# Kernel tuning notes

Measured on AMD Instinct MI355X. Metric: run time of the kernel, lower is better.

Reference implementation:

```python
import jax, jax.numpy as jnp
import numpy as np

V, L, H, D = 2048, 16, 8, 64   # vocab, max_chars, n_head, word_vec_d
B = 8192                        # number of words in batch (rows of char_code)
NW_TOTAL = 8192                 # len(word_code)
N_NAMES = 2048                  # total names (4 words each)
N_GROUPS = 8                    # groups of names (256 each)
PAD = 0
TEMP = D ** 0.5
LN_EPS = 1e-5


def make_pos():
    freq = D // 2
    inv = 1.0 / np.power(10000.0, np.arange(freq) / freq)
    ph = np.outer(np.arange(L), inv)
    return jnp.asarray(np.hstack([np.cos(ph), np.sin(ph)]).astype(np.float32))


def setup_inputs() -> dict:
    key = jax.random.key(0)
    ks = jax.random.split(key, 8)
    char_emb = jax.random.normal(ks[0], (V, D), jnp.float32) * 0.02
    char_emb = char_emb.at[PAD].set(0.0)  # padding_idx row
    Wc = jax.random.normal(ks[1], (D, 3 * H * D), jnp.float32) * 0.02
    bc = jnp.zeros((3 * H * D,), jnp.float32)
    Wp = jax.random.normal(ks[2], (D, 3 * H * D), jnp.float32) * 0.02
    bp = jnp.zeros((3 * H * D,), jnp.float32)
    gamma = jnp.ones((D,), jnp.float32)
    beta = jnp.zeros((D,), jnp.float32)
    W1 = jax.random.normal(ks[3], (H, 16), jnp.float32) * 0.1
    b1 = jnp.zeros((16,), jnp.float32)
    W2 = jax.random.normal(ks[4], (16, 8), jnp.float32) * 0.1
    b2 = jnp.zeros((8,), jnp.float32)
    char_code = jax.random.randint(ks[5], (B, L), 1, V)
    char_code = char_code.at[::4, -2:].set(PAD)  # some padded tails
    word_code = jax.random.randint(ks[6], (NW_TOTAL,), 0, B)
    n_words = np.full((N_NAMES,), NW_TOTAL // N_NAMES, dtype=np.int64)
    n_names = np.full((N_GROUPS,), N_NAMES // N_GROUPS, dtype=np.int64)
    return {"char_emb": char_emb, "Wc": Wc, "bc": bc, "Wp": Wp, "bp": bp,
            "gamma": gamma, "beta": beta, "W1": W1, "b1": b1, "W2": W2, "b2": b2,
            "char_code": char_code, "word_code": word_code,
            "n_words": n_words, "n_names": n_names}


def reference(char_emb, Wc, bc, Wp, bp, gamma, beta, W1, b1, W2, b2,
              char_code, word_code, n_words, n_names):
    pos = make_pos()
    # ComputeQKV: linear d -> 3*H*d, reshape [N,3,H,D]
    cqkv = (char_emb @ Wc + bc).reshape(V, 3, H, D)
    cq, ck, cv = cqkv[:, 0], cqkv[:, 1], cqkv[:, 2]        # [V,H,D]
    pqkv = (pos @ Wp + bp).reshape(L, 3, H, D)
    pq, pk, pv = pqkv[:, 0], pqkv[:, 1], pqkv[:, 2]        # [L,H,D]
    # precomputed score tables
    char_qk = jnp.einsum('xhd,yhd->hxy', cq, ck).at[:, :, PAD].set(-1e9)  # [H,V,V]
    pos_qk = jnp.einsum('xhd,yhd->hxy', pq, pk)                            # [H,L,L]
    # char_q@pos_k + (pos_q@char_k)^T summed over the first dim of char_pos_qk
    cp = jnp.einsum('vhd,lhd->hvl', cq, pk) + jnp.einsum('lhd,vhd->hvl', pq, ck)  # [H,V,L]
    code = char_code                                        # [B,L]
    # gather-assembled scores, no [H,B*L,V] intermediate
    sim = (char_qk[:, code[:, :, None], code[:, None, :]]   # [H,B,L,L]
           + cp[:, code]
           + pos_qk[:, None]) / TEMP
    attn = jax.nn.softmax(sim, axis=-1)                     # [H,B,L,L] (dropout=0)
    v = jnp.transpose(cv[code], (2, 0, 1, 3)) + pv.transpose(1, 0, 2)[:, None]  # [H,B,L,D]
    out = jnp.einsum('hbij,hbjd->bihd', attn, v)            # [B,L,H,D]
    mu = out.mean(-1, keepdims=True)
    var = out.var(-1, keepdims=True)
    out = (out - mu) / jnp.sqrt(var + LN_EPS) * gamma + beta  # LayerNorm(D)
    char_ft = jnp.transpose(out, (0, 2, 1, 3))              # [B,H,L,D]
    mask = (code != PAD)
    pooled = jnp.einsum('bl,bhld->bhd', mask.astype(out.dtype), char_ft) \
             / mask.sum(-1)[:, None, None]                  # masked mean over chars
    x = jnp.transpose(pooled, (0, 2, 1))                    # [B,D,H]
    x = jax.nn.relu(x @ W1 + b1) @ W2 + b2                  # MLP over head dim -> [B,D,8]
    word_ft = x.reshape(B, -1)[word_code]                   # [NW_TOTAL, D*8]
    nw = np.asarray(n_words)
    seg = jnp.asarray(np.repeat(np.arange(nw.size), nw))
    name_ft = jax.ops.segment_sum(word_ft, seg, num_segments=nw.size) \
              / jnp.asarray(nw, word_ft.dtype)[:, None]     # ragged mean -> [N_NAMES, D*8]
    splits = np.cumsum(np.asarray(n_names))[:-1]
    return tuple(jnp.split(name_ft, splits, axis=0))
```

## Files before the change

kernel.cpp:

```cpp
#include <hip/hip_runtime.h>
#include <hip/hip_bf16.h>
#include <math.h>

typedef __attribute__((ext_vector_type(8))) short bfrag;
typedef __attribute__((ext_vector_type(4))) float ffrag;
typedef __attribute__((ext_vector_type(4))) float f4v;
typedef __attribute__((ext_vector_type(2))) float f2v;

#define C3 1536
#define PS 24
#define VS 136

__device__ __forceinline__ unsigned short f2bf(float f) {
    unsigned u = __float_as_uint(f);
    return (unsigned short)((u + 0x7FFFu + ((u >> 16) & 1u)) >> 16);
}
__device__ __forceinline__ float bf2f(unsigned short u) {
    return __uint_as_float((unsigned)u << 16);
}

__device__ __forceinline__ float row16_sum(float x) {
    int v;
    v = __builtin_amdgcn_update_dpp(0, __float_as_int(x), 0xB1, 0xF, 0xF, true);
    x += __int_as_float(v);
    v = __builtin_amdgcn_update_dpp(0, __float_as_int(x), 0x4E, 0xF, 0xF, true);
    x += __int_as_float(v);
    v = __builtin_amdgcn_update_dpp(0, __float_as_int(x), 0x124, 0xF, 0xF, true);
    x += __int_as_float(v);
    v = __builtin_amdgcn_update_dpp(0, __float_as_int(x), 0x128, 0xF, 0xF, true);
    x += __int_as_float(v);
    return x;
}

__global__ __launch_bounds__(256) void precompute_kernel(
    const float* __restrict__ char_emb, const float* __restrict__ Wc, const float* __restrict__ bc,
    const float* __restrict__ Wp, const float* __restrict__ bp,
    const float* __restrict__ gamma, const float* __restrict__ beta,
    unsigned short* __restrict__ cqkv, unsigned short* __restrict__ pbf,
    unsigned short* __restrict__ pvb, float* __restrict__ gbtab)
{
    const int b = blockIdx.x;
    const int t = threadIdx.x;
    if (b < 1536) {
        const int mt = b / 6;
        const int nt = b - mt * 6;
        const int m0 = mt * 8;
        const int c = nt * 256 + t;
        const float qs = (c < 512) ? 0.125f : 1.f;
        const float bias = bc[c];
        float acc[8];
        #pragma unroll
        for (int r = 0; r < 8; ++r) acc[r] = bias;
        #pragma unroll 16
        for (int dd = 0; dd < 64; ++dd) {
            const float wv = Wc[dd * C3 + c];
            #pragma unroll
            for (int r = 0; r < 8; ++r)
                acc[r] = fmaf(char_emb[(m0 + r) * 64 + dd], wv, acc[r]);
        }
        #pragma unroll
        for (int r = 0; r < 8; ++r)
            cqkv[(size_t)(m0 + r) * C3 + c] = f2bf(acc[r] * qs);
    } else {
        const int e = b - 1536;
        const int l = e / 6;
        const int cc = e - l * 6;
        if (b == 1536 && t < 64) {
            #pragma unroll
            for (int dt = 0; dt < 4; ++dt) {
                gbtab[t * 8 + dt]     = gamma[dt * 16 + t];
                gbtab[t * 8 + 4 + dt] = beta[dt * 16 + t];
            }
        }
        __shared__ float spos[64];
        if (t < 64) {
            const int f = t & 31;
            const float inv = exp2f(-(float)f * 0.41524101186092034f);
            const float ph = (float)l * inv;
            spos[t] = (t < 32) ? cosf(ph) : sinf(ph);
        }
        __syncthreads();
        const int c = t + cc * 256;
        float acc = bp[c];
        #pragma unroll
        for (int dd = 0; dd < 64; ++dd)
            acc = fmaf(spos[dd], Wp[dd * C3 + c], acc);
        if (c < 1024) {
            const float qs = (c < 512) ? 0.125f : 1.f;
            pbf[(c >> 6) * 1024 + l * 64 + (c & 63)] = f2bf(acc * qs);
        } else {
            const int h = (c >> 6) & 7, d = c & 63;
            pvb[((h * 4 + (d >> 4)) * 2 + (l >> 3)) * 128 + (d & 15) * 8 + (l & 7)] = f2bf(acc);
        }
    }
}

__global__ __launch_bounds__(256) void cp_kernel(
    const unsigned short* __restrict__ cqkv, const unsigned short* __restrict__ pbf,
    float* __restrict__ cps, float* __restrict__ pqk)
{
    const int b = blockIdx.x;
    const int t = threadIdx.x;
    if (b < 256) {
        const int lane = t & 63, wid = t >> 6;
        const int quad = lane >> 4, n = lane & 15;
        const int h = b >> 5;
        const int v0 = (b & 31) * 64 + wid * 16;
        const unsigned short* arow = cqkv + (size_t)(v0 + n) * C3 + h * 64;
        const unsigned short* pk = pbf + (8 + h) * 1024 + n * 64;
        const unsigned short* pq = pbf + h * 1024 + n * 64;
        ffrag acc = {0.f, 0.f, 0.f, 0.f};
        #pragma unroll
        for (int s = 0; s < 2; ++s) {
            const bfrag aF = *(const bfrag*)(arow + s * 32 + quad * 8);
            const bfrag bF = *(const bfrag*)(pk + s * 32 + quad * 8);
            acc = __builtin_amdgcn_mfma_f32_16x16x32_bf16(aF, bF, acc, 0, 0, 0);
        }
        #pragma unroll
        for (int s = 0; s < 2; ++s) {
            const bfrag aF = *(const bfrag*)(arow + 512 + s * 32 + quad * 8);
            const bfrag bF = *(const bfrag*)(pq + s * 32 + quad * 8);
            acc = __builtin_amdgcn_mfma_f32_16x16x32_bf16(aF, bF, acc, 0, 0, 0);
        }
        #pragma unroll
        for (int r = 0; r < 4; ++r)
            cps[((size_t)h * 2048 + v0 + quad * 4 + r) * 16 + n] = acc[r];
    } else {
        #pragma unroll
        for (int i = 0; i < 8; ++i) {
            const int e = t * 8 + i;
            const int h = e >> 8, r = (e >> 4) & 15, c = e & 15;
            const unsigned short* pq = pbf + h * 1024 + r * 64;
            const unsigned short* pk = pbf + (8 + h) * 1024 + c * 64;
            float s = 0.f;
            #pragma unroll
            for (int c8 = 0; c8 < 8; ++c8) {
                const bfrag a = *(const bfrag*)(pq + c8 * 8);
                const bfrag bb = *(const bfrag*)(pk + c8 * 8);
                #pragma unroll
                for (int j = 0; j < 8; ++j)
                    s += bf2f((unsigned short)a[j]) * bf2f((unsigned short)bb[j]);
            }
            pqk[e] = s;
        }
    }
}

__global__ __launch_bounds__(256, 7) void attn_kernel(
    const unsigned short* __restrict__ cqkv,
    const unsigned short* __restrict__ pvb, const int* __restrict__ char_code,
    const float* __restrict__ gbtab,
    const float* __restrict__ cps, const float* __restrict__ pqk,
    float* __restrict__ pooled)
{
    __shared__ __attribute__((aligned(16))) unsigned short sVt[4 * 8 * VS];
    __shared__ __attribute__((aligned(16))) unsigned short sP[4 * 16 * PS];

    const int t = threadIdx.x;
    const int lane = t & 63;
    const int wid = t >> 6;
    const int h = blockIdx.x & 7;
    const int w = (blockIdx.x >> 3) * 4 + wid;
    const int quad = lane >> 4;
    const int n = lane & 15;
    const int q2 = quad & 1;

    const int code = char_code[w * 16 + n];
    const bool kvalid = (code != 0);
    const unsigned long long msk = __ballot(kvalid);
    const int nv = __popcll(msk & 0xFFFFull);

    int rc[4];
    #pragma unroll
    for (int rr = 0; rr < 4; ++rr) rc[rr] = __shfl(code, quad * 4 + rr);

    const f4v g4 = *(const f4v*)(gbtab + n * 8);
    const f4v b4 = *(const f4v*)(gbtab + n * 8 + 4);

    unsigned short* vt = sVt + wid * 8 * VS;
    unsigned short* pt = sP + wid * 16 * PS;

    bfrag onesf;
    #pragma unroll
    for (int j = 0; j < 8; ++j) onesf[j] = (short)0x3F80;

    const unsigned short* cvp = cqkv + (size_t)code * C3 + 1024 + h * 64;
    #pragma unroll
    for (int cc = 0; cc < 2; ++cc) {
        const int d8 = quad + cc * 4;
        const bfrag cv = *(const bfrag*)(cvp + d8 * 8);
        #pragma unroll
        for (int j = 0; j < 8; ++j) {
            const int d = d8 * 8 + j;
            const int e = ((d >> 4) * 2 + (n >> 3)) * VS
                        + ((d & 15) ^ ((n >> 3) << 2)) * 8 + (n & 7);
            vt[e] = (unsigned short)cv[j];
        }
    }

    const float* cph = cps + (size_t)h * 32768;
    const float* pqh = pqk + h * 256;
    ffrag accS;
    #pragma unroll
    for (int rr = 0; rr < 4; ++rr)
        accS[rr] = cph[rc[rr] * 16 + n] + pqh[(quad * 4 + rr) * 16 + n];
    const unsigned short* cbase = cqkv + (size_t)code * C3 + h * 64;
    #pragma unroll
    for (int cc = 0; cc < 2; ++cc) {
        const int off = quad * 8 + cc * 32;
        const bfrag cqF = *(const bfrag*)(cbase + off);
        const bfrag ckF = *(const bfrag*)(cbase + 512 + off);
        accS = __builtin_amdgcn_mfma_f32_16x16x32_bf16(cqF, ckF, accS, 0, 0, 0);
    }

    #pragma unroll
    for (int r = 0; r < 4; ++r) {
        const float pr = kvalid ? __expf(accS[r]) : 0.f;
        pt[(quad * 4 + r) * PS + n] = f2bf(pr);
    }

    bfrag ap;
    #pragma unroll
    for (int j = 0; j < 8; ++j) ap[j] = 0;
    if (quad < 2) ap = *(const bfrag*)(pt + n * PS + quad * 8);
    ffrag accO[4];
    #pragma unroll
    for (int dt = 0; dt < 4; ++dt) { ffrag z = {0.f,0.f,0.f,0.f}; accO[dt] = z; }
    #pragma unroll
    for (int dt = 0; dt < 4; ++dt) {
        const bfrag bcv = *(const bfrag*)(vt + (dt * 2 + q2) * VS + (n ^ (q2 << 2)) * 8);
        accO[dt] = __builtin_amdgcn_mfma_f32_16x16x32_bf16(ap, bcv, accO[dt], 0, 0, 0);
        const bfrag bpv = *(const bfrag*)(pvb + ((h * 4 + dt) * 2 + q2) * 128 + n * 8);
        accO[dt] = __builtin_amdgcn_mfma_f32_16x16x32_bf16(ap, bpv, accO[dt], 0, 0, 0);
    }
    ffrag accE = {0.f, 0.f, 0.f, 0.f};
    accE = __builtin_amdgcn_mfma_f32_16x16x32_bf16(ap, onesf, accE, 0, 0, 0);

    float ps1[4], ps2[4];
    #pragma unroll
    for (int r = 0; r < 4; ++r) {
        ps1[r] = accO[0][r] + accO[1][r] + accO[2][r] + accO[3][r];
        ps2[r] = accO[0][r]*accO[0][r] + accO[1][r]*accO[1][r]
               + accO[2][r]*accO[2][r] + accO[3][r]*accO[3][r];
        ps1[r] = row16_sum(ps1[r]);
        ps2[r] = row16_sum(ps2[r]);
    }
    float pool[4] = {0.f, 0.f, 0.f, 0.f};
    #pragma unroll
    for (int r = 0; r < 4; ++r) {
        const float mu   = ps1[r] * 0.015625f;
        const float var  = fmaxf(ps2[r] * 0.015625f - mu * mu, 0.f);
        const float rstd = rsqrtf(var + accE[r] * accE[r] * 1e-5f);
        const float iv = ((msk >> (quad * 4 + r)) & 1ull) ? 1.f : 0.f;
        #pragma unroll
        for (int dt = 0; dt < 4; ++dt)
            pool[dt] += iv * fmaf((accO[dt][r] - mu) * rstd, g4[dt], b4[dt]);
    }
    #pragma unroll
    for (int xm = 16; xm <= 32; xm <<= 1) {
        #pragma unroll
        for (int dt = 0; dt < 4; ++dt) pool[dt] += __shfl_xor(pool[dt], xm);
    }
    if (quad == 0) {
        const float invnv = 1.f / (float)nv;
        f4v res;
        #pragma unroll
        for (int dt = 0; dt < 4; ++dt) res[dt] = pool[dt] * invnv;
        *(f4v*)(pooled + (size_t)w * 512 + h * 64 + n * 4) = res;
    }
}

__global__ __launch_bounds__(256) void name_mlp_avg_kernel(
    const float* __restrict__ pooled, const int* __restrict__ word_code,
    const int* __restrict__ n_words,
    const float* __restrict__ W1, const float* __restrict__ b1,
    const float* __restrict__ W2, const float* __restrict__ b2,
    float* __restrict__ out)
{
    __shared__ float sWb[280];
    const int t = threadIdx.x;
    const int lane = t & 63;
    const int nm = blockIdx.x * 4 + (t >> 6);

    if (t < 128) { sWb[t] = W1[t]; sWb[144 + t] = W2[t]; }
    else if (t < 144) sWb[t] = b1[t - 128];
    else if (t < 152) sWb[272 + (t - 144)] = b2[t - 144];
    __syncthreads();

    int part = 0;
    for (int i = lane; i < nm; i += 64) part += n_words[i];
    #pragma unroll
    for (int xm = 1; xm <= 32; xm <<= 1) part += __shfl_xor(part, xm);
    const int off = part;
    const int cnt = n_words[nm];

    const int pidx = (lane & 15) * 4 + (lane >> 4);
    float a[8];
    #pragma unroll
    for (int o = 0; o < 8; ++o) a[o] = 0.f;

    for (int r = 0; r < cnt; ++r) {
        const int wc = word_code[off + r];
        const float* pr = pooled + (size_t)wc * 512 + pidx;
        float pl[8];
        #pragma unroll
        for (int hh = 0; hh < 8; ++hh) pl[hh] = pr[hh * 64];
        #pragma unroll
        for (int c = 0; c < 16; ++c) {
            float hs = sWb[128 + c];
            #pragma unroll
            for (int hh = 0; hh < 8; ++hh) hs = fmaf(pl[hh], sWb[hh * 16 + c], hs);
            hs = fmaxf(hs, 0.f);
            #pragma unroll
            for (int o = 0; o < 8; ++o) a[o] = fmaf(hs, sWb[144 + c * 8 + o], a[o]);
        }
    }
    const float inv = 1.f / (float)cnt;
    f4v r0, r1;
    #pragma unroll
    for (int o = 0; o < 4; ++o) { r0[o] = a[o] * inv + sWb[272 + o]; }
    #pragma unroll
    for (int o = 0; o < 4; ++o) { r1[o] = a[4 + o] * inv + sWb[276 + o]; }
    *(f4v*)(out + (size_t)nm * 512 + lane * 8) = r0;
    *(f4v*)(out + (size_t)nm * 512 + lane * 8 + 4) = r1;
}

extern "C" void kernel_launch(void* const* d_in, const int* in_sizes, int n_in,
                              void* d_out, int out_size, void* d_ws, size_t ws_size,
                              hipStream_t stream) {
    (void)in_sizes; (void)n_in; (void)out_size; (void)ws_size;
    const float* char_emb = (const float*)d_in[0];
    const float* Wc    = (const float*)d_in[1];
    const float* bc    = (const float*)d_in[2];
    const float* Wp    = (const float*)d_in[3];
    const float* bp    = (const float*)d_in[4];
    const float* gamma = (const float*)d_in[5];
    const float* beta  = (const float*)d_in[6];
    const float* W1    = (const float*)d_in[7];
    const float* b1    = (const float*)d_in[8];
    const float* W2    = (const float*)d_in[9];
    const float* b2    = (const float*)d_in[10];
    const int* char_code = (const int*)d_in[11];
    const int* word_code = (const int*)d_in[12];
    const int* n_words   = (const int*)d_in[13];

    char* ws = (char*)d_ws;
    unsigned short* cqkv = (unsigned short*)ws;
    unsigned short* pbf  = (unsigned short*)(ws + 6291456);
    unsigned short* pvb  = (unsigned short*)(ws + 6324224);
    float* pooled = (float*)(ws + 6340608);
    float* gbtab = (float*)(ws + 23117824);
    float* cps   = (float*)(ws + 23119872);
    float* pqk   = (float*)(ws + 24168448);
    float* out = (float*)d_out;

    precompute_kernel<<<1632, 256, 0, stream>>>(char_emb, Wc, bc, Wp, bp, gamma, beta,
                                                cqkv, pbf, pvb, gbtab);
    cp_kernel<<<257, 256, 0, stream>>>(cqkv, pbf, cps, pqk);
    attn_kernel<<<16384, 256, 0, stream>>>(cqkv, pvb, char_code, gbtab, cps, pqk, pooled);
    name_mlp_avg_kernel<<<512, 256, 0, stream>>>(pooled, word_code, n_words,
                                                 W1, b1, W2, b2, out);
}
```

Measured before the change: 192.7 us.

## Compute transposed score tile in attention to vectorize bias loads and P stores

The attention kernel swaps the MFMA operands so each lane holds a transposed score tile. The per-row bias terms can then be read as contiguous float4 loads from cps and pqk instead of four scattered gathers that needed shuffled codes. The softmax numerators are packed with v_cvt_pk_bf16_f32 and written as one 8-byte LDS store, and the key mask is applied multiplicatively and reused for pooling. The pos-pos score part of cp_kernel is also split across 8 blocks instead of 1, spreading that serial tail work.

```diff
diff --git a/kernel.cpp b/kernel.cpp
--- a/kernel.cpp
+++ b/kernel.cpp
@@ -6,6 +6,7 @@
 typedef __attribute__((ext_vector_type(4))) float ffrag;
 typedef __attribute__((ext_vector_type(4))) float f4v;
 typedef __attribute__((ext_vector_type(2))) float f2v;
+typedef __attribute__((ext_vector_type(2))) unsigned u2v;
 
 #define C3 1536
 #define PS 24
@@ -126,23 +127,20 @@
         for (int r = 0; r < 4; ++r)
             cps[((size_t)h * 2048 + v0 + quad * 4 + r) * 16 + n] = acc[r];
     } else {
-        #pragma unroll
-        for (int i = 0; i < 8; ++i) {
-            const int e = t * 8 + i;
-            const int h = e >> 8, r = (e >> 4) & 15, c = e & 15;
-            const unsigned short* pq = pbf + h * 1024 + r * 64;
-            const unsigned short* pk = pbf + (8 + h) * 1024 + c * 64;
-            float s = 0.f;
-            #pragma unroll
-            for (int c8 = 0; c8 < 8; ++c8) {
-                const bfrag a = *(const bfrag*)(pq + c8 * 8);
-                const bfrag bb = *(const bfrag*)(pk + c8 * 8);
-                #pragma unroll
-                for (int j = 0; j < 8; ++j)
-                    s += bf2f((unsigned short)a[j]) * bf2f((unsigned short)bb[j]);
-            }
-            pqk[e] = s;
-        }
+        const int e = (b - 256) * 256 + t;
+        const int h = e >> 8, r = (e >> 4) & 15, c = e & 15;
+        const unsigned short* pq = pbf + h * 1024 + r * 64;
+        const unsigned short* pk = pbf + (8 + h) * 1024 + c * 64;
+        float s = 0.f;
+        #pragma unroll
+        for (int c8 = 0; c8 < 8; ++c8) {
+            const bfrag a = *(const bfrag*)(pq + c8 * 8);
+            const bfrag bb = *(const bfrag*)(pk + c8 * 8);
+            #pragma unroll
+            for (int j = 0; j < 8; ++j)
+                s += bf2f((unsigned short)a[j]) * bf2f((unsigned short)bb[j]);
+        }
+        pqk[e] = s;
     }
 }
 
@@ -170,9 +168,10 @@
     const unsigned long long msk = __ballot(kvalid);
     const int nv = __popcll(msk & 0xFFFFull);
 
-    int rc[4];
-    #pragma unroll
-    for (int rr = 0; rr < 4; ++rr) rc[rr] = __shfl(code, quad * 4 + rr);
+    float mrow[4];
+    #pragma unroll
+    for (int r = 0; r < 4; ++r)
+        mrow[r] = ((msk >> (quad * 4 + r)) & 1ull) ? 1.f : 0.f;
 
     const f4v g4 = *(const f4v*)(gbtab + n * 8);
     const f4v b4 = *(const f4v*)(gbtab + n * 8 + 4);
@@ -198,26 +197,29 @@
         }
     }
 
-    const float* cph = cps + (size_t)h * 32768;
-    const float* pqh = pqk + h * 256;
-    ffrag accS;
-    #pragma unroll
-    for (int rr = 0; rr < 4; ++rr)
-        accS[rr] = cph[rc[rr] * 16 + n] + pqh[(quad * 4 + rr) * 16 + n];
+    const f4v c4 = *(const f4v*)(cps + (size_t)h * 32768 + code * 16 + quad * 4);
+    const f4v p4 = *(const f4v*)(pqk + h * 256 + n * 16 + quad * 4);
+    ffrag accST;
+    #pragma unroll
+    for (int r = 0; r < 4; ++r) accST[r] = c4[r] + p4[r];
     const unsigned short* cbase = cqkv + (size_t)code * C3 + h * 64;
     #pragma unroll
     for (int cc = 0; cc < 2; ++cc) {
         const int off = quad * 8 + cc * 32;
         const bfrag cqF = *(const bfrag*)(cbase + off);
         const bfrag ckF = *(const bfrag*)(cbase + 512 + off);
-        accS = __builtin_amdgcn_mfma_f32_16x16x32_bf16(cqF, ckF, accS, 0, 0, 0);
-    }
-
-    #pragma unroll
-    for (int r = 0; r < 4; ++r) {
-        const float pr = kvalid ? __expf(accS[r]) : 0.f;
-        pt[(quad * 4 + r) * PS + n] = f2bf(pr);
-    }
+        accST = __builtin_amdgcn_mfma_f32_16x16x32_bf16(ckF, cqF, accST, 0, 0, 0);
+    }
+
+    const float pr0 = mrow[0] * __expf(accST[0]);
+    const float pr1 = mrow[1] * __expf(accST[1]);
+    const float pr2 = mrow[2] * __expf(accST[2]);
+    const float pr3 = mrow[3] * __expf(accST[3]);
+    unsigned d0, d1;
+    asm("v_cvt_pk_bf16_f32 %0, %1, %2" : "=v"(d0) : "v"(pr0), "v"(pr1));
+    asm("v_cvt_pk_bf16_f32 %0, %1, %2" : "=v"(d1) : "v"(pr2), "v"(pr3));
+    u2v pw; pw[0] = d0; pw[1] = d1;
+    *(u2v*)(pt + n * PS + quad * 4) = pw;
 
     bfrag ap;
     #pragma unroll
@@ -251,10 +253,9 @@
         const float mu   = ps1[r] * 0.015625f;
         const float var  = fmaxf(ps2[r] * 0.015625f - mu * mu, 0.f);
         const float rstd = rsqrtf(var + accE[r] * accE[r] * 1e-5f);
-        const float iv = ((msk >> (quad * 4 + r)) & 1ull) ? 1.f : 0.f;
         #pragma unroll
         for (int dt = 0; dt < 4; ++dt)
-            pool[dt] += iv * fmaf((accO[dt][r] - mu) * rstd, g4[dt], b4[dt]);
+            pool[dt] += mrow[r] * fmaf((accO[dt][r] - mu) * rstd, g4[dt], b4[dt]);
     }
     #pragma unroll
     for (int xm = 16; xm <= 32; xm <<= 1) {
@@ -356,7 +357,7 @@
 
     precompute_kernel<<<1632, 256, 0, stream>>>(char_emb, Wc, bc, Wp, bp, gamma, beta,
                                                 cqkv, pbf, pvb, gbtab);
-    cp_kernel<<<257, 256, 0, stream>>>(cqkv, pbf, cps, pqk);
+    cp_kernel<<<264, 256, 0, stream>>>(cqkv, pbf, cps, pqk);
     attn_kernel<<<16384, 256, 0, stream>>>(cqkv, pvb, char_code, gbtab, cps, pqk, pooled);
     name_mlp_avg_kernel<<<512, 256, 0, stream>>>(pooled, word_code, n_words,
                                                  W1, b1, W2, b2, out);
```

New measurement: 194.0 us. No clear change (+0.7%).
